# Performance work log

Measured on AMD Instinct MI355X. Metric: run time of the kernel, lower is better.

The kernel has to match this reference:

```python
import jax, jax.numpy as jnp
import numpy as np

DIN = 4096
DOUT = 12288
NUM_GATES = DOUT // 3
OFFSET = 1
BS = 4096
Z = 1.0

# fixed 3x5 combine matrix from the module
M = jnp.array([[1., 0., 0., 0., 0.],
               [0., 0., 1., 1., -1.],
               [0., 1., 0., -1., 1.]], dtype=jnp.float32)


def _make_connections():
    g = np.arange(NUM_GATES, dtype=np.int64)
    starts = (g * 3 + OFFSET) % DIN
    conn = (starts[:, None] + np.arange(3, dtype=np.int64)[None, :]) % DIN
    return jnp.asarray(conn, dtype=jnp.int32)


def setup_inputs() -> dict:
    key = jax.random.key(0)
    kx, kw = jax.random.split(key)
    x = jax.random.normal(kx, (BS, DIN), dtype=jnp.float32)
    wgts = jax.random.normal(kw, (NUM_GATES, 3, 4), dtype=jnp.float32)
    connections = _make_connections()
    return {"x": x, "wgts": wgts, "connections": connections}


def reference(x, wgts, connections):
    bs = x.shape[0]
    # gather 3 inputs per gate: [bs, G, 3]
    gathered = x[:, connections]
    # append constant z -> [bs, G, 4]
    zcol = jnp.full((bs, NUM_GATES, 1), Z, dtype=x.dtype)
    inp = jnp.concatenate([gathered, zcol], axis=-1)
    # softmax-weighted small matmul (training path): [G,3,4] x [bs,G,4] -> [bs,G,3]
    wp = jax.nn.softmax(wgts, axis=-1)
    s = jnp.einsum('gik,bgk->bgi', wp, inp)
    # elementwise products -> [bs, G, 5]
    v4 = s[..., 0] * s[..., 1]
    v5 = s[..., 0] * s[..., 2]
    feats = jnp.concatenate([s, v4[..., None], v5[..., None]], axis=-1)
    # fixed 3x5 combine: [bs, G, 3]
    signals = jnp.einsum('rk,bgk->bgr', M, feats)
    # strided slice ::3 on last dim (size 3) keeps only index 0 -> [bs, G]
    out = signals[:, :, ::3].reshape(bs, -1)
    return out
```

## Files before the change

kernel.cpp:

```cpp
#include <hip/hip_runtime.h>

#define DIN  4096
#define NG   4096
#define BS   4096
#define RPB  8
#define BT   1024
#define WROW 4112

typedef float v4f __attribute__((ext_vector_type(4)));

__global__ __launch_bounds__(BT) void fredkin_s0_dbuf(
    const float* __restrict__ x,
    const float* __restrict__ wgts,
    float* __restrict__ out)
{
    __shared__ float xs[2][WROW];

    const int tid = threadIdx.x;
    const int g0  = 4 * tid;

    float4 w[4];
#pragma unroll
    for (int j = 0; j < 4; ++j) {
        float4 r = *reinterpret_cast<const float4*>(wgts + (size_t)(g0 + j) * 12);
        float m  = fmaxf(fmaxf(r.x, r.y), fmaxf(r.z, r.w));
        float e0 = __expf(r.x - m);
        float e1 = __expf(r.y - m);
        float e2 = __expf(r.z - m);
        float e3 = __expf(r.w - m);
        float inv = 1.0f / (e0 + e1 + e2 + e3);
        w[j] = make_float4(e0 * inv, e1 * inv, e2 * inv, e3 * inv);
    }

    const int lb = (12 * tid) & (DIN - 1);

    const int brow = blockIdx.x * RPB;
    const float* xr   = x   + (size_t)brow * DIN + 4 * tid;
    float*       orow = out + (size_t)brow * NG + g0;

    float4 v = *reinterpret_cast<const float4*>(xr);

    for (int r = 0; r < RPB; ++r) {
        float* buf = xs[r & 1];
        *reinterpret_cast<float4*>(&buf[4 * tid]) = v;
        if (tid < 4)
            *reinterpret_cast<float4*>(&buf[DIN + 4 * tid]) = v;

        if (r + 1 < RPB)
            v = *reinterpret_cast<const float4*>(xr + DIN);

        __syncthreads();

        float4 f0 = *reinterpret_cast<const float4*>(&buf[lb]);
        float4 f1 = *reinterpret_cast<const float4*>(&buf[lb + 4]);
        float4 f2 = *reinterpret_cast<const float4*>(&buf[lb + 8]);
        float  e12 = buf[lb + 12];

        v4f o;
        o.x = fmaf(w[0].x, f0.y, fmaf(w[0].y, f0.z, fmaf(w[0].z, f0.w, w[0].w)));
        o.y = fmaf(w[1].x, f1.x, fmaf(w[1].y, f1.y, fmaf(w[1].z, f1.z, w[1].w)));
        o.z = fmaf(w[2].x, f1.w, fmaf(w[2].y, f2.x, fmaf(w[2].z, f2.y, w[2].w)));
        o.w = fmaf(w[3].x, f2.z, fmaf(w[3].y, f2.w, fmaf(w[3].z, e12, w[3].w)));

        __builtin_nontemporal_store(o, reinterpret_cast<v4f*>(orow));

        xr   += DIN;
        orow += NG;
    }
}

extern "C" void kernel_launch(void* const* d_in, const int* in_sizes, int n_in,
                              void* d_out, int out_size, void* d_ws, size_t ws_size,
                              hipStream_t stream) {
    const float* x    = (const float*)d_in[0];
    const float* wgts = (const float*)d_in[1];
    float* out = (float*)d_out;

    fredkin_s0_dbuf<<<dim3(BS / RPB), dim3(BT), 0, stream>>>(x, wgts, out);
}
```

Baseline: 124.4 us.

## Give each wave a private LDS slice to replace block barriers with wave barriers

```diff
diff --git a/kernel.cpp b/kernel.cpp
--- a/kernel.cpp
+++ b/kernel.cpp
@@ -5,21 +5,25 @@
 #define BS   4096
 #define RPB  8
 #define BT   1024
-#define WROW 4112
+#define WSL  768
 
 typedef float v4f __attribute__((ext_vector_type(4)));
 
-__global__ __launch_bounds__(BT) void fredkin_s0_dbuf(
+__global__ __launch_bounds__(BT, 8) void fredkin_s0_wsync(
     const float* __restrict__ x,
     const float* __restrict__ wgts,
     float* __restrict__ out)
 {
-    __shared__ float xs[2][WROW];
+    __shared__ float xs[16 * WSL];
 
     const int tid = threadIdx.x;
-    const int g0  = 4 * tid;
+    const int w   = tid >> 6;
+    const int l   = tid & 63;
+    float* buf = &xs[w * WSL];
 
-    float4 w[4];
+    const int g0 = 256 * w + 4 * l;
+
+    float4 wq[4];
 #pragma unroll
     for (int j = 0; j < 4; ++j) {
         float4 r = *reinterpret_cast<const float4*>(wgts + (size_t)(g0 + j) * 12);
@@ -29,40 +33,59 @@
         float e2 = __expf(r.z - m);
         float e3 = __expf(r.w - m);
         float inv = 1.0f / (e0 + e1 + e2 + e3);
-        w[j] = make_float4(e0 * inv, e1 * inv, e2 * inv, e3 * inv);
+        wq[j] = make_float4(e0 * inv, e1 * inv, e2 * inv, e3 * inv);
     }
 
-    const int lb = (12 * tid) & (DIN - 1);
+    const int wb = (768 * w) & (DIN - 1);
+    const int o0 = (wb + 4 * l)       & (DIN - 1);
+    const int o1 = (wb + 4 * l + 256) & (DIN - 1);
+    const int o2 = (wb + 4 * l + 512) & (DIN - 1);
+    const int ot = (wb + 768)         & (DIN - 1);
 
     const int brow = blockIdx.x * RPB;
-    const float* xr   = x   + (size_t)brow * DIN + 4 * tid;
+    const float* xr   = x   + (size_t)brow * DIN;
     float*       orow = out + (size_t)brow * NG + g0;
 
-    float4 v = *reinterpret_cast<const float4*>(xr);
+    v4f a0 = *reinterpret_cast<const v4f*>(xr + o0);
+    v4f a1 = *reinterpret_cast<const v4f*>(xr + o1);
+    v4f a2 = *reinterpret_cast<const v4f*>(xr + o2);
+    float at = xr[ot];
+
+    const int lb = 12 * l;
 
     for (int r = 0; r < RPB; ++r) {
-        float* buf = xs[r & 1];
-        *reinterpret_cast<float4*>(&buf[4 * tid]) = v;
-        if (tid < 4)
-            *reinterpret_cast<float4*>(&buf[DIN + 4 * tid]) = v;
+        *reinterpret_cast<v4f*>(&buf[4 * l])       = a0;
+        *reinterpret_cast<v4f*>(&buf[4 * l + 256]) = a1;
+        *reinterpret_cast<v4f*>(&buf[4 * l + 512]) = a2;
 
-        if (r + 1 < RPB)
-            v = *reinterpret_cast<const float4*>(xr + DIN);
+        const float tail = at;
 
-        __syncthreads();
+        if (r + 1 < RPB) {
+            const float* xn = xr + DIN;
+            a0 = *reinterpret_cast<const v4f*>(xn + o0);
+            a1 = *reinterpret_cast<const v4f*>(xn + o1);
+            a2 = *reinterpret_cast<const v4f*>(xn + o2);
+            at = xn[ot];
+        }
+
+        __builtin_amdgcn_wave_barrier();
 
         float4 f0 = *reinterpret_cast<const float4*>(&buf[lb]);
         float4 f1 = *reinterpret_cast<const float4*>(&buf[lb + 4]);
         float4 f2 = *reinterpret_cast<const float4*>(&buf[lb + 8]);
-        float  e12 = buf[lb + 12];
+
+        float e12 = __shfl_down(f0.x, 1);
+        if (l == 63) e12 = tail;
 
         v4f o;
-        o.x = fmaf(w[0].x, f0.y, fmaf(w[0].y, f0.z, fmaf(w[0].z, f0.w, w[0].w)));
-        o.y = fmaf(w[1].x, f1.x, fmaf(w[1].y, f1.y, fmaf(w[1].z, f1.z, w[1].w)));
-        o.z = fmaf(w[2].x, f1.w, fmaf(w[2].y, f2.x, fmaf(w[2].z, f2.y, w[2].w)));
-        o.w = fmaf(w[3].x, f2.z, fmaf(w[3].y, f2.w, fmaf(w[3].z, e12, w[3].w)));
+        o.x = fmaf(wq[0].x, f0.y, fmaf(wq[0].y, f0.z, fmaf(wq[0].z, f0.w, wq[0].w)));
+        o.y = fmaf(wq[1].x, f1.x, fmaf(wq[1].y, f1.y, fmaf(wq[1].z, f1.z, wq[1].w)));
+        o.z = fmaf(wq[2].x, f1.w, fmaf(wq[2].y, f2.x, fmaf(wq[2].z, f2.y, wq[2].w)));
+        o.w = fmaf(wq[3].x, f2.z, fmaf(wq[3].y, f2.w, fmaf(wq[3].z, e12, wq[3].w)));
 
         __builtin_nontemporal_store(o, reinterpret_cast<v4f*>(orow));
+
+        __builtin_amdgcn_wave_barrier();
 
         xr   += DIN;
         orow += NG;
@@ -76,5 +99,5 @@
     const float* wgts = (const float*)d_in[1];
     float* out = (float*)d_out;
 
-    fredkin_s0_dbuf<<<dim3(BS / RPB), dim3(BT), 0, stream>>>(x, wgts, out);
+    fredkin_s0_wsync<<<dim3(BS / RPB), dim3(BT), 0, stream>>>(x, wgts, out);
 }
```

Result: no change. 125.1 us (+0.6%).

## Stream x rows into LDS via direct global-to-LDS DMA with 4-stage pipeline

Applied to the files above, without the earlier changes.

```diff
diff --git a/kernel.cpp b/kernel.cpp
--- a/kernel.cpp
+++ b/kernel.cpp
@@ -1,25 +1,34 @@
 #include <hip/hip_runtime.h>
 
-#define DIN  4096
-#define NG   4096
-#define BS   4096
-#define RPB  8
-#define BT   1024
-#define WROW 4112
+#define DIN 4096
+#define NG  4096
+#define BS  4096
+#define RPB 8
+#define BT  1024
 
 typedef float v4f __attribute__((ext_vector_type(4)));
 
-__global__ __launch_bounds__(BT) void fredkin_s0_dbuf(
+#define WAITVM(N) __builtin_amdgcn_s_waitcnt((N) | 0x0F70)
+
+__device__ __forceinline__ void dma16(const float* g, float* lds) {
+    __builtin_amdgcn_global_load_lds(
+        (const __attribute__((address_space(1))) void*)g,
+        (__attribute__((address_space(3))) void*)lds, 16, 0, 0);
+}
+
+__global__ __launch_bounds__(BT, 8) void fredkin_s0_dma(
     const float* __restrict__ x,
     const float* __restrict__ wgts,
     float* __restrict__ out)
 {
-    __shared__ float xs[2][WROW];
+    __shared__ float B0[DIN], B1[DIN], B2[DIN], B3[DIN];
 
     const int tid = threadIdx.x;
+    const int w   = tid >> 6;
+    const int l   = tid & 63;
     const int g0  = 4 * tid;
 
-    float4 w[4];
+    float4 wq[4];
 #pragma unroll
     for (int j = 0; j < 4; ++j) {
         float4 r = *reinterpret_cast<const float4*>(wgts + (size_t)(g0 + j) * 12);
@@ -29,44 +38,52 @@
         float e2 = __expf(r.z - m);
         float e3 = __expf(r.w - m);
         float inv = 1.0f / (e0 + e1 + e2 + e3);
-        w[j] = make_float4(e0 * inv, e1 * inv, e2 * inv, e3 * inv);
+        wq[j] = make_float4(e0 * inv, e1 * inv, e2 * inv, e3 * inv);
     }
 
+    const int brow = blockIdx.x * RPB;
+    const float* xb   = x   + (size_t)brow * DIN;
+    float*       orow = out + (size_t)brow * NG + g0;
+    const int doff = 256 * w + 4 * l;
+
     const int lb = (12 * tid) & (DIN - 1);
+    const int i1 = (lb + 4)  & (DIN - 1);
+    const int i2 = (lb + 8)  & (DIN - 1);
+    const int i3 = (lb + 12) & (DIN - 1);
 
-    const int brow = blockIdx.x * RPB;
-    const float* xr   = x   + (size_t)brow * DIN + 4 * tid;
-    float*       orow = out + (size_t)brow * NG + g0;
+    dma16(xb + 0 * DIN + doff, B0 + 256 * w);
+    dma16(xb + 1 * DIN + doff, B1 + 256 * w);
+    dma16(xb + 2 * DIN + doff, B2 + 256 * w);
 
-    float4 v = *reinterpret_cast<const float4*>(xr);
+#define FRED_ITER(R, NWAIT, RBUF, WBUF, DO_DMA)                                     \
+    {                                                                               \
+        asm volatile("" ::: "memory");                                              \
+        WAITVM(NWAIT);                                      \
+        __builtin_amdgcn_s_barrier();             \
+        asm volatile("" ::: "memory");                                              \
+        if (DO_DMA) dma16(xb + (size_t)(R + 3) * DIN + doff, WBUF + 256 * w);       \
+        float4 f0 = *reinterpret_cast<const float4*>(&RBUF[lb]);       \
+        float4 f1 = *reinterpret_cast<const float4*>(&RBUF[i1]);       \
+        float4 f2 = *reinterpret_cast<const float4*>(&RBUF[i2]);       \
+        float e12 = __shfl_down(f0.x, 1);             \
+        if (l == 63) e12 = RBUF[i3];              \
+        v4f o;                                                                      \
+        o.x = fmaf(wq[0].x, f0.y, fmaf(wq[0].y, f0.z, fmaf(wq[0].z, f0.w, wq[0].w))); \
+        o.y = fmaf(wq[1].x, f1.x, fmaf(wq[1].y, f1.y, fmaf(wq[1].z, f1.z, wq[1].w))); \
+        o.z = fmaf(wq[2].x, f1.w, fmaf(wq[2].y, f2.x, fmaf(wq[2].z, f2.y, wq[2].w))); \
+        o.w = fmaf(wq[3].x, f2.z, fmaf(wq[3].y, f2.w, fmaf(wq[3].z, e12, wq[3].w))); \
+        __builtin_nontemporal_store(o, reinterpret_cast<v4f*>(orow + (size_t)(R) * NG)); \
+    }
 
-    for (int r = 0; r < RPB; ++r) {
-        float* buf = xs[r & 1];
-        *reinterpret_cast<float4*>(&buf[4 * tid]) = v;
-        if (tid < 4)
-            *reinterpret_cast<float4*>(&buf[DIN + 4 * tid]) = v;
-
-        if (r + 1 < RPB)
-            v = *reinterpret_cast<const float4*>(xr + DIN);
-
-        __syncthreads();
-
-        float4 f0 = *reinterpret_cast<const float4*>(&buf[lb]);
-        float4 f1 = *reinterpret_cast<const float4*>(&buf[lb + 4]);
-        float4 f2 = *reinterpret_cast<const float4*>(&buf[lb + 8]);
-        float  e12 = buf[lb + 12];
-
-        v4f o;
-        o.x = fmaf(w[0].x, f0.y, fmaf(w[0].y, f0.z, fmaf(w[0].z, f0.w, w[0].w)));
-        o.y = fmaf(w[1].x, f1.x, fmaf(w[1].y, f1.y, fmaf(w[1].z, f1.z, w[1].w)));
-        o.z = fmaf(w[2].x, f1.w, fmaf(w[2].y, f2.x, fmaf(w[2].z, f2.y, w[2].w)));
-        o.w = fmaf(w[3].x, f2.z, fmaf(w[3].y, f2.w, fmaf(w[3].z, e12, w[3].w)));
-
-        __builtin_nontemporal_store(o, reinterpret_cast<v4f*>(orow));
-
-        xr   += DIN;
-        orow += NG;
-    }
+    FRED_ITER(0, 2, B0, B3, 1)
+    FRED_ITER(1, 3, B1, B0, 1)
+    FRED_ITER(2, 4, B2, B1, 1)
+    FRED_ITER(3, 5, B3, B2, 1)
+    FRED_ITER(4, 5, B0, B3, 1)
+    FRED_ITER(5, 5, B1, B0, 0)
+    FRED_ITER(6, 4, B2, B1, 0)
+    FRED_ITER(7, 3, B3, B2, 0)
+#undef FRED_ITER
 }
 
 extern "C" void kernel_launch(void* const* d_in, const int* in_sizes, int n_in,
@@ -76,5 +93,5 @@
     const float* wgts = (const float*)d_in[1];
     float* out = (float*)d_out;
 
-    fredkin_s0_dbuf<<<dim3(BS / RPB), dim3(BT), 0, stream>>>(x, wgts, out);
+    fredkin_s0_dma<<<dim3(BS / RPB), dim3(BT), 0, stream>>>(x, wgts, out);
 }
```

Result: faster. 116.3 us (-6.5%).
